# Optimization experiments

Hardware: AMD Instinct MI355X
Metric: run time of the kernel (lower is better)

Reference implementation:

```python
import jax, jax.numpy as jnp
import numpy as np

D_MODEL = 256
NHEAD = 8
HEAD_DIM = D_MODEL // NHEAD
NLAYERS = 8
LAYER_NAMES = ('self', 'cross', 'self', 'cross', 'self', 'cross', 'self', 'cross')
LN_EPS = 1e-5
ATTN_EPS = 1e-6


def _layernorm(x, g, b):
    mu = jnp.mean(x, axis=-1, keepdims=True)
    var = jnp.mean(jnp.square(x - mu), axis=-1, keepdims=True)
    return (x - mu) * jax.lax.rsqrt(var + LN_EPS) * g + b


def _encoder_layer(x, source, Wq, Wk, Wv, Wm, W1, W2, g1, b1, g2, b2):
    # x: [N, L, C], source: [N, S, C]; weights stored [in, out] so y = x @ W
    bs, L, C = x.shape
    S = source.shape[1]
    q = (x @ Wq).reshape(bs, L, NHEAD, HEAD_DIM)
    k = (source @ Wk).reshape(bs, S, NHEAD, HEAD_DIM)
    v = (source @ Wv).reshape(bs, S, NHEAD, HEAD_DIM)
    # LoFTR LinearAttention: feature map elu(x)+1, O(N d^2) kernelized attention
    Q = jax.nn.elu(q) + 1.0
    K = jax.nn.elu(k) + 1.0
    v_n = v / S  # normalize values by kv length for numerical stability
    KV = jnp.einsum('nshd,nshv->nhdv', K, v_n)            # [N,H,D,D]
    Z = 1.0 / (jnp.einsum('nlhd,nhd->nlh', Q, K.sum(axis=1)) + ATTN_EPS)
    msg = jnp.einsum('nlhd,nhdv,nlh->nlhv', Q, KV, Z) * S  # [N,L,H,D]
    msg = msg.reshape(bs, L, C) @ Wm
    msg = _layernorm(msg, g1, b1)
    h = jnp.concatenate([x, msg], axis=-1)                 # [N,L,2C]
    h = jax.nn.relu(h @ W1) @ W2
    h = _layernorm(h, g2, b2)
    return x + h


def _transformer(feat0, feat1, Wq, Wk, Wv, Wm, W1, W2, g1, b1, g2, b2):
    for i, name in enumerate(LAYER_NAMES):
        p = (Wq[i], Wk[i], Wv[i], Wm[i], W1[i], W2[i], g1[i], b1[i], g2[i], b2[i])
        if name == 'self':
            feat0 = _encoder_layer(feat0, feat0, *p)
            feat1 = _encoder_layer(feat1, feat1, *p)
        else:  # cross
            new0 = _encoder_layer(feat0, feat1, *p)
            feat1 = _encoder_layer(feat1, feat0, *p)
            feat0 = new0
    return feat0, feat1


def setup_inputs() -> dict:
    key = jax.random.key(0)
    ks = jax.random.split(key, 8)
    N, L = 4, 4800
    feat0 = jax.random.normal(ks[0], (N, L, D_MODEL), jnp.float32)
    feat1 = jax.random.normal(ks[1], (N, L, D_MODEL), jnp.float32)
    xav = lambda k, fi, fo: jax.random.normal(k, (NLAYERS, fi, fo), jnp.float32) * float(np.sqrt(2.0 / (fi + fo)))
    Wq = xav(ks[2], D_MODEL, D_MODEL)
    Wk = xav(ks[3], D_MODEL, D_MODEL)
    Wv = xav(ks[4], D_MODEL, D_MODEL)
    Wm = xav(ks[5], D_MODEL, D_MODEL)
    W1 = xav(ks[6], 2 * D_MODEL, 2 * D_MODEL)
    W2 = xav(ks[7], 2 * D_MODEL, D_MODEL)
    g1 = jnp.ones((NLAYERS, D_MODEL), jnp.float32)
    b1 = jnp.zeros((NLAYERS, D_MODEL), jnp.float32)
    g2 = jnp.ones((NLAYERS, D_MODEL), jnp.float32)
    b2 = jnp.zeros((NLAYERS, D_MODEL), jnp.float32)
    return dict(feat0=feat0, feat1=feat1, Wq=Wq, Wk=Wk, Wv=Wv, Wm=Wm,
                W1=W1, W2=W2, g1=g1, b1=b1, g2=g2, b2=b2)


def reference(feat0, feat1, Wq, Wk, Wv, Wm, W1, W2, g1, b1, g2, b2):
    return _transformer(feat0, feat1, Wq, Wk, Wv, Wm, W1, W2, g1, b1, g2, b2)
```

## Files before the change

### kernel.cpp

```cpp
#include <hip/hip_runtime.h>
#include <math.h>

#define RTOT 19200
#define RALL 38400
#define CDIM 256
#define SLEN 4800
#define NB 8
#define NHEAD 8
#define SEG 25
#define SCHUNK 192

typedef __attribute__((ext_vector_type(8))) short short8v;
typedef __attribute__((ext_vector_type(4))) float f32x4;

__device__ __forceinline__ ushort f2b(float f) {
    unsigned u = __float_as_uint(f);
    unsigned r = (u + 0x7FFFu + ((u >> 16) & 1u)) >> 16;
    return (ushort)r;
}
__device__ __forceinline__ float b2f(ushort u) {
    return __uint_as_float(((unsigned)u) << 16);
}

__device__ __forceinline__ float elu1(float v) { return v > 0.0f ? v + 1.0f : __expf(v); }

__device__ __forceinline__ void gload16(const void* g, void* l) {
    __builtin_amdgcn_global_load_lds((const __attribute__((address_space(1))) void*)g,
                                     (__attribute__((address_space(3))) void*)l, 16, 0, 0);
}

__global__ __launch_bounds__(256) void qkv_gemm(
    const ushort* __restrict__ A, const ushort* __restrict__ Bt,
    ushort* __restrict__ Oq, ushort* __restrict__ Ok, ushort* __restrict__ Ov)
{
    __shared__ __align__(16) ushort As[2][128 * 32];
    __shared__ __align__(16) ushort Bs[2][128 * 32];
    const int t = threadIdx.x;
    const int wave = t >> 6, lane = t & 63;
    const int bm = blockIdx.y * 128, bn = blockIdx.x * 128;
    const int wr = wave >> 1, wc = wave & 1;
    const int lr = lane & 15, lk = (lane >> 4) * 8;

    const int srow = t >> 2;
    const int sgrp = ((t & 3) * 8) ^ ((srow & 3) * 8);
    const ushort* bAr = A + (size_t)(bm + srow) * 256 + sgrp;
    const ushort* bBr = Bt + (size_t)(bn + srow) * 256 + sgrp;

    const f32x4 z4 = {0.f, 0.f, 0.f, 0.f};
    f32x4 acc[4][4];
    #pragma unroll
    for (int m = 0; m < 4; ++m)
        #pragma unroll
        for (int n = 0; n < 4; ++n) acc[m][n] = z4;

    auto stage = [&](int k0, int b) {
        char* la = (char*)As[b] + wave * 1024;
        char* lb = (char*)Bs[b] + wave * 1024;
        gload16(bAr + k0, la);
        gload16(bAr + k0 + 64 * 256, la + 4096);
        gload16(bBr + k0, lb);
        gload16(bBr + k0 + 64 * 256, lb + 4096);
    };

    stage(0, 0);
    __syncthreads();
    int cur = 0;
    for (int k0 = 0; k0 < 256; k0 += 32) {
        if (k0 + 32 < 256) stage(k0 + 32, cur ^ 1);
        short8v af[4], bfr[4];
        #pragma unroll
        for (int m = 0; m < 4; ++m) {
            const int r = wr * 64 + m * 16 + lr;
            af[m] = *(const short8v*)&As[cur][r * 32 + (lk ^ ((r & 3) * 8))];
        }
        #pragma unroll
        for (int n = 0; n < 4; ++n) {
            const int r = wc * 64 + n * 16 + lr;
            bfr[n] = *(const short8v*)&Bs[cur][r * 32 + (lk ^ ((r & 3) * 8))];
        }
        #pragma unroll
        for (int m = 0; m < 4; ++m)
            #pragma unroll
            for (int n = 0; n < 4; ++n)
                acc[m][n] = __builtin_amdgcn_mfma_f32_16x16x32_bf16(af[m], bfr[n], acc[m][n], 0, 0, 0);
        __syncthreads();
        cur ^= 1;
    }

    const int orow = bm + wr * 64 + (lane >> 4) * 4;
    const int ocol = bn + wc * 64 + lr;
    #pragma unroll
    for (int m = 0; m < 4; ++m)
        #pragma unroll
        for (int n = 0; n < 4; ++n)
            #pragma unroll
            for (int j = 0; j < 4; ++j) {
                const float v = acc[m][n][j];
                const size_t row = (size_t)(orow + m * 16 + j);
                const int col = ocol + n * 16;
                const int seg = col >> 8, c = col & 255;
                ushort* dst = seg == 0 ? Oq : (seg == 1 ? Ok : Ov);
                dst[row * 256 + c] = f2b(seg < 2 ? elu1(v) : v);
            }
}

__global__ __launch_bounds__(256) void attn_wm_ln(
    const ushort* __restrict__ Qb, const ushort* __restrict__ KVbT,
    const ushort* __restrict__ Ksb, const ushort* __restrict__ WmT,
    const float* __restrict__ g, const float* __restrict__ bb,
    ushort* __restrict__ mln, int xorv)
{
    __shared__ __align__(16) ushort Ms[32 * 256];
    __shared__ __align__(16) ushort Bs[2][256 * 32];
    __shared__ float red[2][4][32];
    const int t = threadIdx.x, wave = t >> 6, lane = t & 63;
    const int bm = blockIdx.x * 32;
    const int n = bm / SLEN, src = n ^ xorv;
    const int lr = lane & 15, kg = lane >> 4, lk = kg * 8;
    const f32x4 z4 = {0.f, 0.f, 0.f, 0.f};

    const int srow = t >> 2;
    const int sg = ((t & 3) * 8) ^ ((srow & 3) * 8);
    const ushort* bP = WmT + (size_t)srow * 256 + sg;
    auto stageB = [&](int k0, int b) {
        char* lb = (char*)Bs[b] + wave * 1024;
        gload16(bP + k0, lb);
        gload16(bP + k0 + 64 * 256, lb + 4096);
        gload16(bP + k0 + 128 * 256, lb + 8192);
        gload16(bP + k0 + 192 * 256, lb + 12288);
    };
    stageB(0, 0);

    {
        const int rw = (wave & 1) * 16;
        const size_t qrow = ((size_t)bm + rw + lr) * CDIM;
        char* mb = (char*)Ms;
        for (int h = (wave >> 1); h < NHEAD; h += 2) {
            const short8v af = *(const short8v*)&Qb[qrow + h * 32 + kg * 8];
            const ushort* bbp = KVbT + ((size_t)(src * NHEAD + h)) * 1024;
            const short8v b0 = *(const short8v*)&bbp[lr * 32 + kg * 8];
            const short8v b1 = *(const short8v*)&bbp[(16 + lr) * 32 + kg * 8];
            const short8v bz = *(const short8v*)&Ksb[((size_t)(src * NHEAD + h)) * 512 + lr * 32 + kg * 8];
            f32x4 a0 = __builtin_amdgcn_mfma_f32_16x16x32_bf16(af, b0, z4, 0, 0, 0);
            f32x4 a1 = __builtin_amdgcn_mfma_f32_16x16x32_bf16(af, b1, z4, 0, 0, 0);
            f32x4 az = __builtin_amdgcn_mfma_f32_16x16x32_bf16(af, bz, z4, 0, 0, 0);
            #pragma unroll
            for (int j = 0; j < 4; ++j) {
                const float zj = __shfl(az[j], lane & 48);
                const float rz = 1.0f / (zj + 1e-6f);
                const int orow = rw + kg * 4 + j;
                const int swz = (orow & 7) << 4;
                *(ushort*)(mb + ((orow * 512 + (h * 32 + lr) * 2) ^ swz)) = f2b(a0[j] * rz);
                *(ushort*)(mb + ((orow * 512 + (h * 32 + 16 + lr) * 2) ^ swz)) = f2b(a1[j] * rz);
            }
        }
    }
    __syncthreads();

    f32x4 acc[2][4];
    #pragma unroll
    for (int m = 0; m < 2; ++m)
        #pragma unroll
        for (int nn = 0; nn < 4; ++nn) acc[m][nn] = z4;

    int cur = 0;
    for (int k0 = 0; k0 < 256; k0 += 32) {
        if (k0 + 32 < 256) stageB(k0 + 32, cur ^ 1);
        short8v af[2], bfr[4];
        #pragma unroll
        for (int m = 0; m < 2; ++m) {
            const int r = m * 16 + lr;
            af[m] = *(const short8v*)((char*)Ms + ((r * 512 + k0 * 2 + kg * 16) ^ ((r & 7) << 4)));
        }
        #pragma unroll
        for (int nn = 0; nn < 4; ++nn) {
            const int r = wave * 64 + nn * 16 + lr;
            bfr[nn] = *(const short8v*)&Bs[cur][r * 32 + (lk ^ ((r & 3) * 8))];
        }
        #pragma unroll
        for (int m = 0; m < 2; ++m)
            #pragma unroll
            for (int nn = 0; nn < 4; ++nn)
                acc[m][nn] = __builtin_amdgcn_mfma_f32_16x16x32_bf16(af[m], bfr[nn], acc[m][nn], 0, 0, 0);
        __syncthreads();
        cur ^= 1;
    }

    #pragma unroll
    for (int m = 0; m < 2; ++m)
        #pragma unroll
        for (int j = 0; j < 4; ++j) {
            float s = 0.f, q = 0.f;
            #pragma unroll
            for (int nn = 0; nn < 4; ++nn) { const float v = acc[m][nn][j]; s += v; q += v * v; }
            #pragma unroll
            for (int mk = 1; mk < 16; mk <<= 1) { s += __shfl_xor(s, mk); q += __shfl_xor(q, mk); }
            if (lr == 0) {
                red[0][wave][m * 16 + kg * 4 + j] = s;
                red[1][wave][m * 16 + kg * 4 + j] = q;
            }
        }
    __syncthreads();

    float gv[4], bv[4];
    #pragma unroll
    for (int nn = 0; nn < 4; ++nn) {
        const int col = wave * 64 + nn * 16 + lr;
        gv[nn] = g[col]; bv[nn] = bb[col];
    }
    #pragma unroll
    for (int m = 0; m < 2; ++m)
        #pragma unroll
        for (int j = 0; j < 4; ++j) {
            const int row = m * 16 + kg * 4 + j;
            const float tot = red[0][0][row] + red[0][1][row] + red[0][2][row] + red[0][3][row];
            const float tq  = red[1][0][row] + red[1][1][row] + red[1][2][row] + red[1][3][row];
            const float mu = tot * (1.0f / 256.0f);
            const float var = tq * (1.0f / 256.0f) - mu * mu;
            const float inv = rsqrtf(var + 1e-5f);
            const size_t go = (size_t)(bm + row) * CDIM;
            #pragma unroll
            for (int nn = 0; nn < 4; ++nn) {
                const int col = wave * 64 + nn * 16 + lr;
                mln[go + col] = f2b((acc[m][nn][j] - mu) * inv * gv[nn] + bv[nn]);
            }
        }
}

__global__ __launch_bounds__(256) void mlp_ln(
    const ushort* __restrict__ xb, const ushort* __restrict__ mlnSrc,
    const ushort* __restrict__ W1T, const ushort* __restrict__ W2T,
    const float* __restrict__ g, const float* __restrict__ bb,
    const float* __restrict__ rx0, const float* __restrict__ rx1,
    float* __restrict__ outf, ushort* __restrict__ outb)
{
    __shared__ __align__(16) ushort A512[32 * 512];
    __shared__ __align__(16) ushort Bs[2][256 * 32];
    __shared__ __align__(16) ushort H1[32 * 128];
    __shared__ float red[2][4][32];
    const int t = threadIdx.x, wave = t >> 6, lane = t & 63;
    const int bm = blockIdx.x * 32;
    const int lr = lane & 15, kg = lane >> 4, lk = kg * 8;
    const f32x4 z4 = {0.f, 0.f, 0.f, 0.f};

    {
        const ushort* mln2 = mlnSrc - 256;
        #pragma unroll
        for (int i = 0; i < 8; ++i) {
            const int row = i * 4 + wave;
            const int gl = lane ^ (row & 7);
            const ushort* s = (gl < 32) ? (xb + (size_t)(bm + row) * 256 + gl * 8)
                                        : (mln2 + (size_t)(bm + row) * 256 + gl * 8);
            gload16(s, (char*)A512 + row * 1024);
        }
    }

    const int srow = t >> 2;
    const int sg = ((t & 3) * 8) ^ ((srow & 3) * 8);
    auto stageIdx = [&](int idx, int b) {
        char* lb = (char*)Bs[b] + wave * 1024;
        const int c = idx / 12, s = idx % 12;
        if (s < 8) {
            const ushort* p = W1T + (size_t)(c * 128 + srow) * 512 + s * 64 + sg;
            gload16(p, lb);
            gload16(p + (size_t)64 * 512, lb + 4096);
            gload16(p + 32, lb + 8192);
            gload16(p + (size_t)64 * 512 + 32, lb + 12288);
        } else {
            const ushort* p = W2T + (size_t)srow * 512 + c * 128 + (s - 8) * 32 + sg;
            gload16(p, lb);
            gload16(p + (size_t)64 * 512, lb + 4096);
            gload16(p + (size_t)128 * 512, lb + 8192);
            gload16(p + (size_t)192 * 512, lb + 12288);
        }
    };

    f32x4 acc2[2][4];
    #pragma unroll
    for (int m = 0; m < 2; ++m)
        #pragma unroll
        for (int nn = 0; nn < 4; ++nn) acc2[m][nn] = z4;

    stageIdx(0, 0);
    __syncthreads();
    int cur = 0, sid = 0;

    for (int c = 0; c < 4; ++c) {
        f32x4 acc1[2][2];
        #pragma unroll
        for (int m = 0; m < 2; ++m)
            #pragma unroll
            for (int nn = 0; nn < 2; ++nn) acc1[m][nn] = z4;

        for (int s = 0; s < 8; ++s) {
            if (sid + 1 < 48) stageIdx(sid + 1, cur ^ 1);
            #pragma unroll
            for (int half = 0; half < 2; ++half) {
                short8v af[2], bfr[2];
                #pragma unroll
                for (int m = 0; m < 2; ++m) {
                    const int r = m * 16 + lr;
                    const int q = s * 8 + half * 4 + kg;
                    af[m] = *(const short8v*)((char*)A512 + r * 1024 + ((q ^ (r & 7)) << 4));
                }
                #pragma unroll
                for (int nn = 0; nn < 2; ++nn) {
                    const int r = wave * 32 + nn * 16 + lr;
                    bfr[nn] = *(const short8v*)&Bs[cur][half * 4096 + r * 32 + (lk ^ ((r & 3) * 8))];
                }
                #pragma unroll
                for (int m = 0; m < 2; ++m)
                    #pragma unroll
                    for (int nn = 0; nn < 2; ++nn)
                        acc1[m][nn] = __builtin_amdgcn_mfma_f32_16x16x32_bf16(af[m], bfr[nn], acc1[m][nn], 0, 0, 0);
            }
            __syncthreads();
            cur ^= 1; ++sid;
        }

        #pragma unroll
        for (int m = 0; m < 2; ++m)
            #pragma unroll
            for (int nn = 0; nn < 2; ++nn)
                #pragma unroll
                for (int j = 0; j < 4; ++j) {
                    const int row = m * 16 + kg * 4 + j;
                    const int col = wave * 32 + nn * 16 + lr;
                    const float v = acc1[m][nn][j];
                    const int grp = col >> 3;
                    *(ushort*)((char*)H1 + row * 256 + ((grp ^ (row & 7)) << 4) + (col & 7) * 2)
                        = f2b(v > 0.f ? v : 0.f);
                }
        __syncthreads();

        for (int s = 0; s < 4; ++s) {
            if (sid + 1 < 48) stageIdx(sid + 1, cur ^ 1);
            short8v af[2], bfr[4];
            #pragma unroll
            for (int m = 0; m < 2; ++m) {
                const int r = m * 16 + lr;
                const int q = s * 4 + kg;
                af[m] = *(const short8v*)((char*)H1 + r * 256 + ((q ^ (r & 7)) << 4));
            }
            #pragma unroll
            for (int nn = 0; nn < 4; ++nn) {
                const int r = wave * 64 + nn * 16 + lr;
                bfr[nn] = *(const short8v*)&Bs[cur][r * 32 + (lk ^ ((r & 3) * 8))];
            }
            #pragma unroll
            for (int m = 0; m < 2; ++m)
                #pragma unroll
                for (int nn = 0; nn < 4; ++nn)
                    acc2[m][nn] = __builtin_amdgcn_mfma_f32_16x16x32_bf16(af[m], bfr[nn], acc2[m][nn], 0, 0, 0);
            __syncthreads();
            cur ^= 1; ++sid;
        }
    }

    #pragma unroll
    for (int m = 0; m < 2; ++m)
        #pragma unroll
        for (int j = 0; j < 4; ++j) {
            float s = 0.f, q = 0.f;
            #pragma unroll
            for (int nn = 0; nn < 4; ++nn) { const float v = acc2[m][nn][j]; s += v; q += v * v; }
            #pragma unroll
            for (int mk = 1; mk < 16; mk <<= 1) { s += __shfl_xor(s, mk); q += __shfl_xor(q, mk); }
            if (lr == 0) {
                red[0][wave][m * 16 + kg * 4 + j] = s;
                red[1][wave][m * 16 + kg * 4 + j] = q;
            }
        }
    __syncthreads();

    float gv[4], bv[4];
    #pragma unroll
    for (int nn = 0; nn < 4; ++nn) {
        const int col = wave * 64 + nn * 16 + lr;
        gv[nn] = g[col]; bv[nn] = bb[col];
    }
    const float* rxb = (bm < RTOT) ? rx0 + (size_t)bm * CDIM : rx1 + (size_t)(bm - RTOT) * CDIM;

    #pragma unroll
    for (int m = 0; m < 2; ++m)
        #pragma unroll
        for (int j = 0; j < 4; ++j) {
            const int row = m * 16 + kg * 4 + j;
            const float tot = red[0][0][row] + red[0][1][row] + red[0][2][row] + red[0][3][row];
            const float tq  = red[1][0][row] + red[1][1][row] + red[1][2][row] + red[1][3][row];
            const float mu = tot * (1.0f / 256.0f);
            const float var = tq * (1.0f / 256.0f) - mu * mu;
            const float inv = rsqrtf(var + 1e-5f);
            const size_t go = (size_t)(bm + row) * CDIM;
            #pragma unroll
            for (int nn = 0; nn < 4; ++nn) {
                const int col = wave * 64 + nn * 16 + lr;
                float val = (acc2[m][nn][j] - mu) * inv * gv[nn] + bv[nn];
                val += rxb[(size_t)row * CDIM + col];
                outf[go + col] = val;
                outb[go + col] = f2b(val);
            }
        }
}

__global__ __launch_bounds__(256) void wconv_t(
    const float* __restrict__ src, ushort* __restrict__ dst, int R, int C, size_t dstride)
{
    __shared__ float tile[32][33];
    const int l = blockIdx.z;
    const int r0 = blockIdx.y * 32, c0 = blockIdx.x * 32;
    const int tx = threadIdx.x & 31, ty = threadIdx.x >> 5;
    const float* s = src + (size_t)l * R * C;
    ushort* d = dst + (size_t)l * dstride;
    for (int i = ty; i < 32; i += 8) tile[i][tx] = s[(size_t)(r0 + i) * C + c0 + tx];
    __syncthreads();
    for (int i = ty; i < 32; i += 8) d[(size_t)(c0 + i) * R + r0 + tx] = f2b(tile[tx][i]);
}

__global__ __launch_bounds__(256) void kv_part_k(
    const ushort* __restrict__ Kb, const ushort* __restrict__ Vb,
    float* __restrict__ KVp, float* __restrict__ Ksp)
{
    const int blk = blockIdx.x;
    const int seg = blk % SEG;
    const int h = (blk / SEG) % NHEAD;
    const int n = blk / (SEG * NHEAD);
    const int s0 = seg * SCHUNK;
    __shared__ float Ks[16][32];
    __shared__ float Vs[16][32];
    const int t = threadIdx.x;
    const int rr = t >> 4, c2 = (t & 15) * 2;
    const int d = t >> 3, v0 = (t & 7) * 4;
    float a0 = 0, a1 = 0, a2 = 0, a3 = 0, ksum = 0;
    for (int c = 0; c < SCHUNK; c += 16) {
        const size_t off = ((size_t)(n * SLEN + s0 + c + rr)) * CDIM + h * 32 + c2;
        const ushort2 ku = *(const ushort2*)&Kb[off];
        const ushort2 vu = *(const ushort2*)&Vb[off];
        Ks[rr][c2] = b2f(ku.x); Ks[rr][c2 + 1] = b2f(ku.y);
        Vs[rr][c2] = b2f(vu.x); Vs[rr][c2 + 1] = b2f(vu.y);
        __syncthreads();
        #pragma unroll
        for (int q = 0; q < 16; ++q) {
            const float kd = Ks[q][d];
            a0 += kd * Vs[q][v0 + 0];
            a1 += kd * Vs[q][v0 + 1];
            a2 += kd * Vs[q][v0 + 2];
            a3 += kd * Vs[q][v0 + 3];
        }
        if (t < 32) {
            #pragma unroll
            for (int q = 0; q < 16; ++q) ksum += Ks[q][t];
        }
        __syncthreads();
    }
    float* kvp = KVp + ((size_t)((n * NHEAD + h) * SEG + seg)) * 1024;
    kvp[t * 4 + 0] = a0;
    kvp[t * 4 + 1] = a1;
    kvp[t * 4 + 2] = a2;
    kvp[t * 4 + 3] = a3;
    if (t < 32) Ksp[((size_t)((n * NHEAD + h) * SEG + seg)) * 32 + t] = ksum;
}

__global__ __launch_bounds__(256) void kv_reduce_k(
    const float* __restrict__ KVp, const float* __restrict__ Ksp,
    ushort* __restrict__ KVbT, ushort* __restrict__ Ksb)
{
    const int nh = blockIdx.x;
    const int t = threadIdx.x;
    #pragma unroll
    for (int i = 0; i < 4; ++i) {
        const int idx = t * 4 + i;
        const int v = idx >> 5, d = idx & 31;
        float s = 0;
        for (int seg = 0; seg < SEG; ++seg)
            s += KVp[((size_t)(nh * SEG + seg)) * 1024 + d * 32 + v];
        KVbT[(size_t)nh * 1024 + idx] = f2b(s);
    }
    #pragma unroll
    for (int i = 0; i < 2; ++i) {
        const int idx = t * 2 + i;
        const int c = idx >> 5, d = idx & 31;
        float s = 0;
        if (c == 0)
            for (int seg = 0; seg < SEG; ++seg)
                s += Ksp[((size_t)(nh * SEG + seg)) * 32 + d];
        Ksb[(size_t)nh * 512 + idx] = f2b(s);
    }
}

__global__ __launch_bounds__(256) void cvt_in_k(const float* __restrict__ src, ushort* __restrict__ dst) {
    const size_t i = ((size_t)blockIdx.x * 256 + threadIdx.x) * 4;
    const float4 v = *(const float4*)&src[i];
    ushort4 ob = make_ushort4(f2b(v.x), f2b(v.y), f2b(v.z), f2b(v.w));
    *(ushort4*)&dst[i] = ob;
}

struct Ws {
    float *xf, *KVp, *Ksp;
    ushort *xb, *Qb, *Kb, *Vb, *KVbT, *Ksb;
    ushort *WqkvT, *WmT, *W1T, *W2T;
};

static void layer_pass(const float* rx0, const float* rx1, float* destf, int xorv,
                       const ushort* WqkvT, const ushort* WmT,
                       const ushort* W1T, const ushort* W2T,
                       const float* g1, const float* b1,
                       const float* g2, const float* b2,
                       const Ws& w, hipStream_t stream)
{
    const dim3 blk(256);
    qkv_gemm<<<dim3(6, RALL / 128), blk, 0, stream>>>(w.xb, WqkvT, w.Qb, w.Kb, w.Vb);
    kv_part_k<<<dim3(NB * NHEAD * SEG), blk, 0, stream>>>(w.Kb, w.Vb, w.KVp, w.Ksp);
    kv_reduce_k<<<dim3(NB * NHEAD), blk, 0, stream>>>(w.KVp, w.Ksp, w.KVbT, w.Ksb);
    attn_wm_ln<<<dim3(RALL / 32), blk, 0, stream>>>(
        w.Qb, w.KVbT, w.Ksb, WmT, g1, b1, w.Kb, xorv);
    mlp_ln<<<dim3(RALL / 32), blk, 0, stream>>>(
        w.xb, w.Kb, W1T, W2T, g2, b2, rx0, rx1, destf, w.xb);
}

extern "C" void kernel_launch(void* const* d_in, const int* in_sizes, int n_in,
                              void* d_out, int out_size, void* d_ws, size_t ws_size,
                              hipStream_t stream) {
    (void)in_sizes; (void)n_in; (void)out_size; (void)ws_size;
    const float* f0in = (const float*)d_in[0];
    const float* f1in = (const float*)d_in[1];
    const float* WqA = (const float*)d_in[2];
    const float* WkA = (const float*)d_in[3];
    const float* WvA = (const float*)d_in[4];
    const float* WmA = (const float*)d_in[5];
    const float* W1A = (const float*)d_in[6];
    const float* W2A = (const float*)d_in[7];
    const float* g1A = (const float*)d_in[8];
    const float* b1A = (const float*)d_in[9];
    const float* g2A = (const float*)d_in[10];
    const float* b2A = (const float*)d_in[11];

    float* outf = (float*)d_out;
    const size_t RC = (size_t)RTOT * CDIM;
    const size_t RAC = (size_t)RALL * CDIM;

    float* wsf = (float*)d_ws;
    Ws w;
    w.xf  = wsf;
    w.KVp = w.xf + RAC;
    w.Ksp = w.KVp + (size_t)64 * SEG * 1024;
    ushort* p = (ushort*)(w.Ksp + 64 * SEG * 32);
    w.xb = p;   p += RAC;
    w.Qb = p;   p += RAC;
    w.Kb = p;   p += RAC;
    w.Vb = p;   p += RAC;
    w.KVbT = p; p += 64 * 1024;
    w.Ksb = p;  p += 64 * 512;
    w.WqkvT = p; p += (size_t)8 * 768 * 256;
    w.WmT = p;  p += (size_t)8 * 256 * 256;
    w.W1T = p;  p += (size_t)8 * 512 * 512;
    w.W2T = p;  p += (size_t)8 * 512 * 256;

    const dim3 blk(256);
    wconv_t<<<dim3(8, 8, 8), blk, 0, stream>>>(WqA, w.WqkvT,             256, 256, 768 * 256);
    wconv_t<<<dim3(8, 8, 8), blk, 0, stream>>>(WkA, w.WqkvT + 256 * 256, 256, 256, 768 * 256);
    wconv_t<<<dim3(8, 8, 8), blk, 0, stream>>>(WvA, w.WqkvT + 512 * 256, 256, 256, 768 * 256);
    wconv_t<<<dim3(8, 8, 8), blk, 0, stream>>>(WmA, w.WmT, 256, 256, 65536);
    wconv_t<<<dim3(16, 16, 8), blk, 0, stream>>>(W1A, w.W1T, 512, 512, 262144);
    wconv_t<<<dim3(8, 16, 8), blk, 0, stream>>>(W2A, w.W2T, 512, 256, 131072);

    cvt_in_k<<<dim3(RC / 1024), blk, 0, stream>>>(f0in, w.xb);
    cvt_in_k<<<dim3(RC / 1024), blk, 0, stream>>>(f1in, w.xb + RC);

    for (int l = 0; l < 8; ++l) {
        const int xorv = (l & 1) ? 4 : 0;
        const float* rx0 = (l == 0) ? f0in : w.xf;
        const float* rx1 = (l == 0) ? f1in : w.xf + RC;
        float* destf = (l == 7) ? outf : w.xf;
        layer_pass(rx0, rx1, destf, xorv,
                   w.WqkvT + (size_t)l * 768 * 256,
                   w.WmT + (size_t)l * 65536,
                   w.W1T + (size_t)l * 262144,
                   w.W2T + (size_t)l * 131072,
                   g1A + l * 256, b1A + l * 256, g2A + l * 256, b2A + l * 256,
                   w, stream);
    }
}
```

Baseline: 1.648 ms.

## Split fused MLP kernel into tiled W1 GEMM and W2 GEMM with LayerNorm

Replaces the fused per-32-row MLP kernel, which recomputed the hidden layer in chunks with small 32-row tiles, with two kernels. The first is a 128x128-tiled W1 GEMM with ReLU that writes a bf16 hidden buffer. The second is a 32-row W2 GEMM fused with LayerNorm and the residual add. The aim is better MFMA tile efficiency and less reloading of W1 weights, at the cost of writing and re-reading a 38400x512 bf16 intermediate through global memory plus an extra launch.

```diff
diff --git a/kernel.cpp b/kernel.cpp
--- a/kernel.cpp
+++ b/kernel.cpp
@@ -102,6 +102,187 @@
                 ushort* dst = seg == 0 ? Oq : (seg == 1 ? Ok : Ov);
                 dst[row * 256 + c] = f2b(seg < 2 ? elu1(v) : v);
             }
+}
+
+__global__ __launch_bounds__(256) void w1_gemm(
+    const ushort* __restrict__ A, const ushort* __restrict__ A2,
+    const ushort* __restrict__ Bt, ushort* __restrict__ O)
+{
+    __shared__ __align__(16) ushort As[2][128 * 32];
+    __shared__ __align__(16) ushort Bs[2][128 * 32];
+    const int t = threadIdx.x;
+    const int wave = t >> 6, lane = t & 63;
+    const int bm = blockIdx.y * 128, bn = blockIdx.x * 128;
+    const int wr = wave >> 1, wc = wave & 1;
+    const int lr = lane & 15, lk = (lane >> 4) * 8;
+
+    const int srow = t >> 2;
+    const int sgrp = ((t & 3) * 8) ^ ((srow & 3) * 8);
+    const ushort* bAr = A + (size_t)(bm + srow) * 256 + sgrp;
+    const ushort* bA2r = A2 + (size_t)(bm + srow) * 256 + sgrp;
+    const ushort* bBr = Bt + (size_t)(bn + srow) * 512 + sgrp;
+
+    const f32x4 z4 = {0.f, 0.f, 0.f, 0.f};
+    f32x4 acc[4][4];
+    #pragma unroll
+    for (int m = 0; m < 4; ++m)
+        #pragma unroll
+        for (int n = 0; n < 4; ++n) acc[m][n] = z4;
+
+    auto stage = [&](int k0, int b) {
+        char* la = (char*)As[b] + wave * 1024;
+        char* lb = (char*)Bs[b] + wave * 1024;
+        const ushort* ga = (k0 < 256) ? (bAr + k0) : (bA2r + (k0 - 256));
+        gload16(ga, la);
+        gload16(ga + 64 * 256, la + 4096);
+        gload16(bBr + k0, lb);
+        gload16(bBr + k0 + (size_t)64 * 512, lb + 4096);
+    };
+
+    stage(0, 0);
+    __syncthreads();
+    int cur = 0;
+    for (int k0 = 0; k0 < 512; k0 += 32) {
+        if (k0 + 32 < 512) stage(k0 + 32, cur ^ 1);
+        short8v af[4], bfr[4];
+        #pragma unroll
+        for (int m = 0; m < 4; ++m) {
+            const int r = wr * 64 + m * 16 + lr;
+            af[m] = *(const short8v*)&As[cur][r * 32 + (lk ^ ((r & 3) * 8))];
+        }
+        #pragma unroll
+        for (int n = 0; n < 4; ++n) {
+            const int r = wc * 64 + n * 16 + lr;
+            bfr[n] = *(const short8v*)&Bs[cur][r * 32 + (lk ^ ((r & 3) * 8))];
+        }
+        #pragma unroll
+        for (int m = 0; m < 4; ++m)
+            #pragma unroll
+            for (int n = 0; n < 4; ++n)
+                acc[m][n] = __builtin_amdgcn_mfma_f32_16x16x32_bf16(af[m], bfr[n], acc[m][n], 0, 0, 0);
+        __syncthreads();
+        cur ^= 1;
+    }
+
+    const int orow = bm + wr * 64 + (lane >> 4) * 4;
+    const int ocol = bn + wc * 64 + lr;
+    #pragma unroll
+    for (int m = 0; m < 4; ++m)
+        #pragma unroll
+        for (int n = 0; n < 4; ++n)
+            #pragma unroll
+            for (int j = 0; j < 4; ++j) {
+                const float v = acc[m][n][j];
+                O[(size_t)(orow + m * 16 + j) * 512 + ocol + n * 16] = f2b(v > 0.f ? v : 0.f);
+            }
+}
+
+__global__ __launch_bounds__(256) void gemm_ln32(
+    const ushort* __restrict__ A, int lda,
+    const ushort* __restrict__ Bt,
+    const float* __restrict__ g, const float* __restrict__ bb,
+    const float* __restrict__ rx0, const float* __restrict__ rx1,
+    float* __restrict__ outf, ushort* __restrict__ outb, int K)
+{
+    __shared__ __align__(16) ushort As[2][32 * 32];
+    __shared__ __align__(16) ushort Bs[2][256 * 32];
+    __shared__ float red[2][4][32];
+    const int t = threadIdx.x;
+    const int wave = t >> 6, lane = t & 63;
+    const int bm = blockIdx.x * 32;
+    const int lr = lane & 15, kg = lane >> 4, lk = kg * 8;
+
+    const int srow = t >> 2;
+    const int sg = ((t & 3) * 8) ^ ((srow & 3) * 8);
+    const ushort* aP = A + (size_t)(bm + srow) * lda + sg;
+    const ushort* bP = Bt + (size_t)srow * K + sg;
+    const size_t b64 = (size_t)64 * K;
+
+    auto stage = [&](int k0, int b) {
+        if (srow < 32) gload16(aP + k0, (char*)As[b] + wave * 1024);
+        char* lb = (char*)Bs[b] + wave * 1024;
+        gload16(bP + k0, lb);
+        gload16(bP + k0 + b64, lb + 4096);
+        gload16(bP + k0 + 2 * b64, lb + 8192);
+        gload16(bP + k0 + 3 * b64, lb + 12288);
+    };
+
+    const f32x4 z4 = {0.f, 0.f, 0.f, 0.f};
+    f32x4 acc[2][4];
+    #pragma unroll
+    for (int m = 0; m < 2; ++m)
+        #pragma unroll
+        for (int n = 0; n < 4; ++n) acc[m][n] = z4;
+
+    stage(0, 0);
+    __syncthreads();
+    int cur = 0;
+    for (int k0 = 0; k0 < K; k0 += 32) {
+        if (k0 + 32 < K) stage(k0 + 32, cur ^ 1);
+        short8v af[2], bfr[4];
+        #pragma unroll
+        for (int m = 0; m < 2; ++m) {
+            const int r = m * 16 + lr;
+            af[m] = *(const short8v*)&As[cur][r * 32 + (lk ^ ((r & 3) * 8))];
+        }
+        #pragma unroll
+        for (int n = 0; n < 4; ++n) {
+            const int r = wave * 64 + n * 16 + lr;
+            bfr[n] = *(const short8v*)&Bs[cur][r * 32 + (lk ^ ((r & 3) * 8))];
+        }
+        #pragma unroll
+        for (int m = 0; m < 2; ++m)
+            #pragma unroll
+            for (int n = 0; n < 4; ++n)
+                acc[m][n] = __builtin_amdgcn_mfma_f32_16x16x32_bf16(af[m], bfr[n], acc[m][n], 0, 0, 0);
+        __syncthreads();
+        cur ^= 1;
+    }
+
+    #pragma unroll
+    for (int m = 0; m < 2; ++m)
+        #pragma unroll
+        for (int j = 0; j < 4; ++j) {
+            float s = 0.f, q = 0.f;
+            #pragma unroll
+            for (int n = 0; n < 4; ++n) { const float v = acc[m][n][j]; s += v; q += v * v; }
+            #pragma unroll
+            for (int mk = 1; mk < 16; mk <<= 1) { s += __shfl_xor(s, mk); q += __shfl_xor(q, mk); }
+            if (lr == 0) {
+                red[0][wave][m * 16 + kg * 4 + j] = s;
+                red[1][wave][m * 16 + kg * 4 + j] = q;
+            }
+        }
+    __syncthreads();
+
+    float gv[4], bv[4];
+    #pragma unroll
+    for (int n = 0; n < 4; ++n) {
+        const int col = wave * 64 + n * 16 + lr;
+        gv[n] = g[col]; bv[n] = bb[col];
+    }
+    const float* rxb = (bm < RTOT) ? rx0 + (size_t)bm * CDIM : rx1 + (size_t)(bm - RTOT) * CDIM;
+
+    #pragma unroll
+    for (int m = 0; m < 2; ++m)
+        #pragma unroll
+        for (int j = 0; j < 4; ++j) {
+            const int row = m * 16 + kg * 4 + j;
+            const float tot = red[0][0][row] + red[0][1][row] + red[0][2][row] + red[0][3][row];
+            const float tq  = red[1][0][row] + red[1][1][row] + red[1][2][row] + red[1][3][row];
+            const float mu = tot * (1.0f / 256.0f);
+            const float var = tq * (1.0f / 256.0f) - mu * mu;
+            const float inv = rsqrtf(var + 1e-5f);
+            const size_t go = (size_t)(bm + row) * CDIM;
+            #pragma unroll
+            for (int n = 0; n < 4; ++n) {
+                const int col = wave * 64 + n * 16 + lr;
+                float val = (acc[m][n][j] - mu) * inv * gv[n] + bv[n];
+                val += rxb[(size_t)row * CDIM + col];
+                outf[go + col] = val;
+                outb[go + col] = f2b(val);
+            }
+        }
 }
 
 __global__ __launch_bounds__(256) void attn_wm_ln(
@@ -223,182 +404,6 @@
             for (int nn = 0; nn < 4; ++nn) {
                 const int col = wave * 64 + nn * 16 + lr;
                 mln[go + col] = f2b((acc[m][nn][j] - mu) * inv * gv[nn] + bv[nn]);
-            }
-        }
-}
-
-__global__ __launch_bounds__(256) void mlp_ln(
-    const ushort* __restrict__ xb, const ushort* __restrict__ mlnSrc,
-    const ushort* __restrict__ W1T, const ushort* __restrict__ W2T,
-    const float* __restrict__ g, const float* __restrict__ bb,
-    const float* __restrict__ rx0, const float* __restrict__ rx1,
-    float* __restrict__ outf, ushort* __restrict__ outb)
-{
-    __shared__ __align__(16) ushort A512[32 * 512];
-    __shared__ __align__(16) ushort Bs[2][256 * 32];
-    __shared__ __align__(16) ushort H1[32 * 128];
-    __shared__ float red[2][4][32];
-    const int t = threadIdx.x, wave = t >> 6, lane = t & 63;
-    const int bm = blockIdx.x * 32;
-    const int lr = lane & 15, kg = lane >> 4, lk = kg * 8;
-    const f32x4 z4 = {0.f, 0.f, 0.f, 0.f};
-
-    {
-        const ushort* mln2 = mlnSrc - 256;
-        #pragma unroll
-        for (int i = 0; i < 8; ++i) {
-            const int row = i * 4 + wave;
-            const int gl = lane ^ (row & 7);
-            const ushort* s = (gl < 32) ? (xb + (size_t)(bm + row) * 256 + gl * 8)
-                                        : (mln2 + (size_t)(bm + row) * 256 + gl * 8);
-            gload16(s, (char*)A512 + row * 1024);
-        }
-    }
-
-    const int srow = t >> 2;
-    const int sg = ((t & 3) * 8) ^ ((srow & 3) * 8);
-    auto stageIdx = [&](int idx, int b) {
-        char* lb = (char*)Bs[b] + wave * 1024;
-        const int c = idx / 12, s = idx % 12;
-        if (s < 8) {
-            const ushort* p = W1T + (size_t)(c * 128 + srow) * 512 + s * 64 + sg;
-            gload16(p, lb);
-            gload16(p + (size_t)64 * 512, lb + 4096);
-            gload16(p + 32, lb + 8192);
-            gload16(p + (size_t)64 * 512 + 32, lb + 12288);
-        } else {
-            const ushort* p = W2T + (size_t)srow * 512 + c * 128 + (s - 8) * 32 + sg;
-            gload16(p, lb);
-            gload16(p + (size_t)64 * 512, lb + 4096);
-            gload16(p + (size_t)128 * 512, lb + 8192);
-            gload16(p + (size_t)192 * 512, lb + 12288);
-        }
-    };
-
-    f32x4 acc2[2][4];
-    #pragma unroll
-    for (int m = 0; m < 2; ++m)
-        #pragma unroll
-        for (int nn = 0; nn < 4; ++nn) acc2[m][nn] = z4;
-
-    stageIdx(0, 0);
-    __syncthreads();
-    int cur = 0, sid = 0;
-
-    for (int c = 0; c < 4; ++c) {
-        f32x4 acc1[2][2];
-        #pragma unroll
-        for (int m = 0; m < 2; ++m)
-            #pragma unroll
-            for (int nn = 0; nn < 2; ++nn) acc1[m][nn] = z4;
-
-        for (int s = 0; s < 8; ++s) {
-            if (sid + 1 < 48) stageIdx(sid + 1, cur ^ 1);
-            #pragma unroll
-            for (int half = 0; half < 2; ++half) {
-                short8v af[2], bfr[2];
-                #pragma unroll
-                for (int m = 0; m < 2; ++m) {
-                    const int r = m * 16 + lr;
-                    const int q = s * 8 + half * 4 + kg;
-                    af[m] = *(const short8v*)((char*)A512 + r * 1024 + ((q ^ (r & 7)) << 4));
-                }
-                #pragma unroll
-                for (int nn = 0; nn < 2; ++nn) {
-                    const int r = wave * 32 + nn * 16 + lr;
-                    bfr[nn] = *(const short8v*)&Bs[cur][half * 4096 + r * 32 + (lk ^ ((r & 3) * 8))];
-                }
-                #pragma unroll
-                for (int m = 0; m < 2; ++m)
-                    #pragma unroll
-                    for (int nn = 0; nn < 2; ++nn)
-                        acc1[m][nn] = __builtin_amdgcn_mfma_f32_16x16x32_bf16(af[m], bfr[nn], acc1[m][nn], 0, 0, 0);
-            }
-            __syncthreads();
-            cur ^= 1; ++sid;
-        }
-
-        #pragma unroll
-        for (int m = 0; m < 2; ++m)
-            #pragma unroll
-            for (int nn = 0; nn < 2; ++nn)
-                #pragma unroll
-                for (int j = 0; j < 4; ++j) {
-                    const int row = m * 16 + kg * 4 + j;
-                    const int col = wave * 32 + nn * 16 + lr;
-                    const float v = acc1[m][nn][j];
-                    const int grp = col >> 3;
-                    *(ushort*)((char*)H1 + row * 256 + ((grp ^ (row & 7)) << 4) + (col & 7) * 2)
-                        = f2b(v > 0.f ? v : 0.f);
-                }
-        __syncthreads();
-
-        for (int s = 0; s < 4; ++s) {
-            if (sid + 1 < 48) stageIdx(sid + 1, cur ^ 1);
-            short8v af[2], bfr[4];
-            #pragma unroll
-            for (int m = 0; m < 2; ++m) {
-                const int r = m * 16 + lr;
-                const int q = s * 4 + kg;
-                af[m] = *(const short8v*)((char*)H1 + r * 256 + ((q ^ (r & 7)) << 4));
-            }
-            #pragma unroll
-            for (int nn = 0; nn < 4; ++nn) {
-                const int r = wave * 64 + nn * 16 + lr;
-                bfr[nn] = *(const short8v*)&Bs[cur][r * 32 + (lk ^ ((r & 3) * 8))];
-            }
-            #pragma unroll
-            for (int m = 0; m < 2; ++m)
-                #pragma unroll
-                for (int nn = 0; nn < 4; ++nn)
-                    acc2[m][nn] = __builtin_amdgcn_mfma_f32_16x16x32_bf16(af[m], bfr[nn], acc2[m][nn], 0, 0, 0);
-            __syncthreads();
-            cur ^= 1; ++sid;
-        }
-    }
-
-    #pragma unroll
-    for (int m = 0; m < 2; ++m)
-        #pragma unroll
-        for (int j = 0; j < 4; ++j) {
-            float s = 0.f, q = 0.f;
-            #pragma unroll
-            for (int nn = 0; nn < 4; ++nn) { const float v = acc2[m][nn][j]; s += v; q += v * v; }
-            #pragma unroll
-            for (int mk = 1; mk < 16; mk <<= 1) { s += __shfl_xor(s, mk); q += __shfl_xor(q, mk); }
-            if (lr == 0) {
-                red[0][wave][m * 16 + kg * 4 + j] = s;
-                red[1][wave][m * 16 + kg * 4 + j] = q;
-            }
-        }
-    __syncthreads();
-
-    float gv[4], bv[4];
-    #pragma unroll
-    for (int nn = 0; nn < 4; ++nn) {
-        const int col = wave * 64 + nn * 16 + lr;
-        gv[nn] = g[col]; bv[nn] = bb[col];
-    }
-    const float* rxb = (bm < RTOT) ? rx0 + (size_t)bm * CDIM : rx1 + (size_t)(bm - RTOT) * CDIM;
-
-    #pragma unroll
-    for (int m = 0; m < 2; ++m)
-        #pragma unroll
-        for (int j = 0; j < 4; ++j) {
-            const int row = m * 16 + kg * 4 + j;
-            const float tot = red[0][0][row] + red[0][1][row] + red[0][2][row] + red[0][3][row];
-            const float tq  = red[1][0][row] + red[1][1][row] + red[1][2][row] + red[1][3][row];
-            const float mu = tot * (1.0f / 256.0f);
-            const float var = tq * (1.0f / 256.0f) - mu * mu;
-            const float inv = rsqrtf(var + 1e-5f);
-            const size_t go = (size_t)(bm + row) * CDIM;
-            #pragma unroll
-            for (int nn = 0; nn < 4; ++nn) {
-                const int col = wave * 64 + nn * 16 + lr;
-                float val = (acc2[m][nn][j] - mu) * inv * gv[nn] + bv[nn];
-                val += rxb[(size_t)row * CDIM + col];
-                outf[go + col] = val;
-                outb[go + col] = f2b(val);
             }
         }
 }
@@ -497,7 +502,7 @@
 
 struct Ws {
     float *xf, *KVp, *Ksp;
-    ushort *xb, *Qb, *Kb, *Vb, *KVbT, *Ksb;
+    ushort *xb, *Qb, *Kb, *Vb, *h1b, *KVbT, *Ksb;
     ushort *WqkvT, *WmT, *W1T, *W2T;
 };
 
@@ -514,8 +519,9 @@
     kv_reduce_k<<<dim3(NB * NHEAD), blk, 0, stream>>>(w.KVp, w.Ksp, w.KVbT, w.Ksb);
     attn_wm_ln<<<dim3(RALL / 32), blk, 0, stream>>>(
         w.Qb, w.KVbT, w.Ksb, WmT, g1, b1, w.Kb, xorv);
-    mlp_ln<<<dim3(RALL / 32), blk, 0, stream>>>(
-        w.xb, w.Kb, W1T, W2T, g2, b2, rx0, rx1, destf, w.xb);
+    w1_gemm<<<dim3(4, RALL / 128), blk, 0, stream>>>(w.xb, w.Kb, W1T, w.h1b);
+    gemm_ln32<<<dim3(RALL / 32), blk, 0, stream>>>(
+        w.h1b, 512, W2T, g2, b2, rx0, rx1, destf, w.xb, 512);
 }
 
 extern "C" void kernel_launch(void* const* d_in, const int* in_sizes, int n_in,
@@ -549,6 +555,7 @@
     w.Qb = p;   p += RAC;
     w.Kb = p;   p += RAC;
     w.Vb = p;   p += RAC;
+    w.h1b = p;  p += (size_t)RALL * 512;
     w.KVbT = p; p += 64 * 1024;
     w.Ksb = p;  p += 64 * 512;
     w.WqkvT = p; p += (size_t)8 * 768 * 256;
```

After: 1.439 ms. -12.7%, faster.
